# Kernel optimization log

Hardware: AMD Instinct MI355X
Metric: run time of the kernel (lower is better)

Reference implementation:

```python
import jax, jax.numpy as jnp
import numpy as np

EMBED = 1024
B, S = 8, 2048

def setup_inputs() -> dict:
    key = jax.random.key(0)
    k1, k2 = jax.random.split(key)
    x = jax.random.normal(k1, (B, S, EMBED), dtype=jnp.float32)
    # torch Linear(embed, 3*embed): store weight already transposed as [E, 3E]
    W_qkv = jax.random.normal(k2, (EMBED, 3 * EMBED), dtype=jnp.float32) * (1.0 / np.sqrt(EMBED))
    b_qkv = jnp.zeros((3 * EMBED,), dtype=jnp.float32)
    return {"x": x, "W_qkv": W_qkv, "b_qkv": b_qkv}

def reference(x, W_qkv, b_qkv):
    E = x.shape[-1]
    qkv = x @ W_qkv + b_qkv                      # [B,S,3E]
    Q, K, V = jnp.split(qkv, 3, axis=-1)         # each [B,S,E]
    scale = 1.0 / jnp.sqrt(jnp.asarray(E, x.dtype))
    scores = jnp.einsum('bqe,bke->bqk', Q, K) * scale  # [B,S,S]
    attn = jax.nn.softmax(scores, axis=-1)
    return jnp.einsum('bqk,bke->bqe', attn, V)   # [B,S,E]
```

## Files before the change

kernel.cpp:

```cpp
#include <hip/hip_runtime.h>

typedef unsigned short u16;
typedef unsigned int u32;
typedef __attribute__((ext_vector_type(8))) short short8;
typedef __attribute__((ext_vector_type(4))) short short4v;
typedef __attribute__((ext_vector_type(4))) float f32x4;

__device__ __forceinline__ u16 f2bf(float f) {
    u32 u = __float_as_uint(f);
    u32 r = (u + 0x7fffu + ((u >> 16) & 1u)) >> 16;
    return (u16)r;
}
__device__ __forceinline__ float bf2f(u16 h) {
    return __uint_as_float(((u32)h) << 16);
}

__device__ __forceinline__ void gload_lds16(const void* g, void* l) {
    __builtin_amdgcn_global_load_lds((const __attribute__((address_space(1))) void*)g,
                                     (__attribute__((address_space(3))) void*)l, 16, 0, 0);
}

#define BARRIER() do { __builtin_amdgcn_sched_barrier(0); __builtin_amdgcn_s_barrier(); __builtin_amdgcn_sched_barrier(0); } while (0)
#define VMCNT(N)  asm volatile("s_waitcnt vmcnt(" #N ")" ::: "memory")

#define STAGE(ptr, LDG, LOFF, RBASE, kelem) \
    do { gload_lds16((ptr) + (size_t)(RBASE) * (LDG) + (kelem),        lds + (LOFF) + ((RBASE) + (wid << 3)) * 128); \
         gload_lds16((ptr) + (size_t)((RBASE) + 64) * (LDG) + (kelem), lds + (LOFF) + ((RBASE) + 64 + (wid << 3)) * 128); } while (0)

template<int ROFF, int QH>
__device__ __forceinline__ void ld_a(short8 (&a)[4][2], const char* lds, int arow, int c0, int c1) {
    #pragma unroll
    for (int mf = 0; mf < 4; ++mf) {
        a[mf][0] = *(const short8*)(lds + ROFF + QH * 16384 + mf * 2048 + arow + c0);
        a[mf][1] = *(const short8*)(lds + ROFF + QH * 16384 + mf * 2048 + arow + c1);
    }
}
template<int ROFF, int QH>
__device__ __forceinline__ void ld_b(short8 (&b)[2][2], const char* lds, int brow, int c0, int c1) {
    #pragma unroll
    for (int nf = 0; nf < 2; ++nf) {
        b[nf][0] = *(const short8*)(lds + ROFF + QH * 16384 + nf * 2048 + brow + c0);
        b[nf][1] = *(const short8*)(lds + ROFF + QH * 16384 + nf * 2048 + brow + c1);
    }
}

template<int QM, int QN>
__device__ __forceinline__ void mfq(f32x4 (&acc)[2][4][2][2], short8 (&a)[4][2], short8 (&b)[2][2]) {
    __builtin_amdgcn_s_setprio(1);
    #pragma unroll
    for (int mf = 0; mf < 4; ++mf)
        #pragma unroll
        for (int nf = 0; nf < 2; ++nf) {
            acc[QM][mf][QN][nf] = __builtin_amdgcn_mfma_f32_16x16x32_bf16(a[mf][0], b[nf][0], acc[QM][mf][QN][nf], 0, 0, 0);
            acc[QM][mf][QN][nf] = __builtin_amdgcn_mfma_f32_16x16x32_bf16(a[mf][1], b[nf][1], acc[QM][mf][QN][nf], 0, 0, 0);
        }
    __builtin_amdgcn_s_setprio(0);
}

template<int EPI, int LDA, int LDB, int LDC, int K>
__global__ __launch_bounds__(512, 2)
void gemm8p(const u16* __restrict__ A, long long sA,
            const u16* __restrict__ B, long long sB,
            void* __restrict__ Cv, long long sC,
            const float* __restrict__ bias, float* __restrict__ ps,
            u16* __restrict__ vt, float scale, int GX, int GY)
{
    extern __shared__ char lds[];
    const int tid  = threadIdx.x;
    const int wid  = tid >> 6;
    const int lane = tid & 63;

    const int nwg = gridDim.x;
    int bid = blockIdx.x;
    bid = (bid & 7) * (nwg >> 3) + (bid >> 3);
    const int bx  = bid % GX;
    const int rem = bid / GX;
    const int by  = rem % GY;
    const long long z = rem / GY;

    const int bm = by * 256, bn = bx * 256;
    const u16* Atile = A + z * sA + (size_t)bm * LDA;
    const u16* Btile = B + z * sB + (size_t)bn * LDB;

    const int wm = wid >> 2, wn = wid & 3;
    const int l15   = lane & 15;
    const int lxor  = (lane & 7) << 4;
    const int khi   = (lane >> 4) << 4;
    const int colk0 = khi ^ lxor;
    const int colk1 = (64 + khi) ^ lxor;
    const int arow  = (wm * 64 + l15) * 128;
    const int brow  = (wn * 32 + l15) * 128;

    const int swz = ((lane & 7) ^ (lane >> 3)) << 3;
    const u16* pA = Atile + (size_t)((wid << 3) + (lane >> 3)) * LDA + swz;
    const u16* pB = Btile + (size_t)((wid << 3) + (lane >> 3)) * LDB + swz;

    f32x4 acc[2][4][2][2];
    #pragma unroll
    for (int i = 0; i < 2; ++i)
        #pragma unroll
        for (int m = 0; m < 4; ++m)
            #pragma unroll
            for (int j = 0; j < 2; ++j)
                #pragma unroll
                for (int n = 0; n < 2; ++n)
                    acc[i][m][j][n] = (f32x4){0.f, 0.f, 0.f, 0.f};

    STAGE(pA, LDA, 0,     0,   0);  STAGE(pA, LDA, 0,     128, 0);
    STAGE(pB, LDB, 32768, 0,   0);  STAGE(pB, LDB, 32768, 128, 0);
    STAGE(pA, LDA, 65536, 0,   64);
    STAGE(pB, LDB, 98304, 0,   64); STAGE(pB, LDB, 98304, 128, 64);
    VMCNT(6);
    BARRIER();

    short8 a[4][2], b0[2][2], b1[2][2];
    const int NI = K >> 7;

    for (int it = 0; it < NI; ++it) {
        const bool more = (it + 1 < NI);
        const int kc1 = it * 128 + 64;
        const int kn  = it * 128 + 128;
        const int kn2 = kn + 64;

        ld_a<0, 0>(a, lds, arow, colk0, colk1);
        ld_b<32768, 0>(b0, lds, brow, colk0, colk1);
        STAGE(pA, LDA, 65536, 128, kc1);
        BARRIER(); mfq<0, 0>(acc, a, b0);
        ld_b<32768, 1>(b1, lds, brow, colk0, colk1);
        BARRIER(); mfq<0, 1>(acc, a, b1);
        ld_a<0, 1>(a, lds, arow, colk0, colk1);
        if (more) STAGE(pB, LDB, 32768, 0, kn);
        BARRIER(); mfq<1, 1>(acc, a, b1);
        if (more) { STAGE(pB, LDB, 32768, 128, kn); VMCNT(4); }
        else      { VMCNT(0); }
        BARRIER(); mfq<1, 0>(acc, a, b0);
        ld_a<65536, 0>(a, lds, arow, colk0, colk1);
        ld_b<98304, 0>(b0, lds, brow, colk0, colk1);
        if (more) STAGE(pA, LDA, 0, 0, kn);
        BARRIER(); mfq<0, 0>(acc, a, b0);
        ld_b<98304, 1>(b1, lds, brow, colk0, colk1);
        if (more) STAGE(pA, LDA, 0, 128, kn);
        BARRIER(); mfq<0, 1>(acc, a, b1);
        ld_a<65536, 1>(a, lds, arow, colk0, colk1);
        if (more) { STAGE(pB, LDB, 98304, 0, kn2); STAGE(pB, LDB, 98304, 128, kn2); }
        BARRIER(); mfq<1, 1>(acc, a, b1);
        if (more) STAGE(pA, LDA, 65536, 0, kn2);
        VMCNT(6);
        BARRIER(); mfq<1, 0>(acc, a, b0);
    }

    const int r0 = (lane >> 4) * 4;
    const int cc = lane & 15;

    if (EPI == 3) {
        BARRIER();
        float* rs = (float*)lds;
        u16* C = (u16*)Cv + z * sC;
        float rsum[2][4][4];
        #pragma unroll
        for (int qm = 0; qm < 2; ++qm)
            #pragma unroll
            for (int mf = 0; mf < 4; ++mf)
                #pragma unroll
                for (int r = 0; r < 4; ++r) rsum[qm][mf][r] = 0.f;
        #pragma unroll
        for (int qn = 0; qn < 2; ++qn)
            #pragma unroll
            for (int nf = 0; nf < 2; ++nf) {
                const int col = bn + qn * 128 + wn * 32 + nf * 16 + cc;
                #pragma unroll
                for (int qm = 0; qm < 2; ++qm)
                    #pragma unroll
                    for (int mf = 0; mf < 4; ++mf) {
                        const int row = bm + qm * 128 + wm * 64 + mf * 16 + r0;
                        #pragma unroll
                        for (int r = 0; r < 4; ++r) {
                            const float e = __expf(acc[qm][mf][qn][nf][r] * scale);
                            const u16 eb = f2bf(e);
                            C[(size_t)(row + r) * LDC + col] = eb;
                            rsum[qm][mf][r] += bf2f(eb);
                        }
                    }
            }
        #pragma unroll
        for (int qm = 0; qm < 2; ++qm)
            #pragma unroll
            for (int mf = 0; mf < 4; ++mf)
                #pragma unroll
                for (int r = 0; r < 4; ++r) {
                    float v = rsum[qm][mf][r];
                    v += __shfl_xor(v, 1); v += __shfl_xor(v, 2);
                    v += __shfl_xor(v, 4); v += __shfl_xor(v, 8);
                    if (cc == 0)
                        rs[wn * 256 + qm * 128 + wm * 64 + mf * 16 + r0 + r] = v;
                }
        __syncthreads();
        if (tid < 256) {
            const float s = rs[tid] + rs[256 + tid] + rs[512 + tid] + rs[768 + tid];
            ps[((size_t)z * 2048 + bm + tid) * GX + bx] = s;
        }
        return;
    }

    if (EPI == 4) {
        BARRIER();
        float* di = (float*)lds;
        if (tid < 256) {
            const float* p = ps + ((size_t)z * 2048 + bm + tid) * 8;
            const float s = ((p[0] + p[1]) + (p[2] + p[3])) + ((p[4] + p[5]) + (p[6] + p[7]));
            di[tid] = 1.0f / s;
        }
        __syncthreads();
        float* C = (float*)Cv + z * sC;
        #pragma unroll
        for (int qn = 0; qn < 2; ++qn)
            #pragma unroll
            for (int nf = 0; nf < 2; ++nf) {
                const int col = bn + qn * 128 + wn * 32 + nf * 16 + cc;
                #pragma unroll
                for (int qm = 0; qm < 2; ++qm)
                    #pragma unroll
                    for (int mf = 0; mf < 4; ++mf) {
                        const int ro = qm * 128 + wm * 64 + mf * 16 + r0;
                        #pragma unroll
                        for (int r = 0; r < 4; ++r)
                            C[(size_t)(bm + ro + r) * LDC + col] = acc[qm][mf][qn][nf][r] * di[ro + r];
                    }
            }
        return;
    }

    if (EPI == 0 && bn >= 2048) {
        #pragma unroll
        for (int qn = 0; qn < 2; ++qn)
            #pragma unroll
            for (int nf = 0; nf < 2; ++nf) {
                const int col = bn + qn * 128 + wn * 32 + nf * 16 + cc;
                const float badd = bias[col];
                const int e = col - 2048;
                #pragma unroll
                for (int qm = 0; qm < 2; ++qm)
                    #pragma unroll
                    for (int mf = 0; mf < 4; ++mf) {
                        const int row = bm + qm * 128 + wm * 64 + mf * 16 + r0;
                        short4v o;
                        #pragma unroll
                        for (int r = 0; r < 4; ++r)
                            o[r] = (short)f2bf(acc[qm][mf][qn][nf][r] + badd);
                        *(short4v*)&vt[((size_t)(row >> 11) << 21) + (size_t)e * 2048 + (row & 2047)] = o;
                    }
            }
        return;
    }

    #pragma unroll
    for (int qn = 0; qn < 2; ++qn)
        #pragma unroll
        for (int nf = 0; nf < 2; ++nf) {
            const int col = bn + qn * 128 + wn * 32 + nf * 16 + cc;
            const float badd = bias[col];
            #pragma unroll
            for (int qm = 0; qm < 2; ++qm)
                #pragma unroll
                for (int mf = 0; mf < 4; ++mf) {
                    const int row = bm + qm * 128 + wm * 64 + mf * 16 + r0;
                    #pragma unroll
                    for (int r = 0; r < 4; ++r) {
                        const float v = acc[qm][mf][qn][nf][r] + badd;
                        ((u16*)Cv + z * sC)[(size_t)(row + r) * LDC + col] = f2bf(v);
                    }
                }
        }
}

__global__ __launch_bounds__(256)
void cvt_fused(const float* __restrict__ x, u16* __restrict__ xb,
               const float* __restrict__ W, u16* __restrict__ Wt)
{
    __shared__ u16 T[32][33];
    const int blk = blockIdx.x;
    const int tid = threadIdx.x;
    if (blk < 4096) {
        const float4* p = (const float4*)x;
        const int i0 = blk * 256 + tid;
        float4 a0 = p[2 * i0],             b0v = p[2 * i0 + 1];
        float4 a1 = p[2 * (i0 + 1048576)], b1v = p[2 * (i0 + 1048576) + 1];
        short8 o0, o1;
        o0[0] = (short)f2bf(a0.x); o0[1] = (short)f2bf(a0.y);
        o0[2] = (short)f2bf(a0.z); o0[3] = (short)f2bf(a0.w);
        o0[4] = (short)f2bf(b0v.x); o0[5] = (short)f2bf(b0v.y);
        o0[6] = (short)f2bf(b0v.z); o0[7] = (short)f2bf(b0v.w);
        o1[0] = (short)f2bf(a1.x); o1[1] = (short)f2bf(a1.y);
        o1[2] = (short)f2bf(a1.z); o1[3] = (short)f2bf(a1.w);
        o1[4] = (short)f2bf(b1v.x); o1[5] = (short)f2bf(b1v.y);
        o1[6] = (short)f2bf(b1v.z); o1[7] = (short)f2bf(b1v.w);
        ((short8*)xb)[i0] = o0;
        ((short8*)xb)[i0 + 1048576] = o1;
        return;
    }
    const int wb = blk - 4096;
    const int c0 = (wb % 96) * 32;
    const int r0 = (wb / 96) * 32;
    const int tr = tid >> 3;
    const int tc = (tid & 7) * 4;
    const float4 v = *(const float4*)&W[(size_t)(r0 + tr) * 3072 + c0 + tc];
    T[tr][tc + 0] = f2bf(v.x); T[tr][tc + 1] = f2bf(v.y);
    T[tr][tc + 2] = f2bf(v.z); T[tr][tc + 3] = f2bf(v.w);
    __syncthreads();
    short4v o;
    o[0] = (short)T[tc + 0][tr]; o[1] = (short)T[tc + 1][tr];
    o[2] = (short)T[tc + 2][tr]; o[3] = (short)T[tc + 3][tr];
    *(short4v*)&Wt[(size_t)(c0 + tr) * 1024 + r0 + tc] = o;
}

extern "C" void kernel_launch(void* const* d_in, const int* in_sizes, int n_in,
                              void* d_out, int out_size, void* d_ws, size_t ws_size,
                              hipStream_t stream) {
    const float* x    = (const float*)d_in[0];
    const float* W    = (const float*)d_in[1];
    const float* bias = (const float*)d_in[2];
    float* out = (float*)d_out;

    const int B = 8, S = 2048, E = 1024, N3 = 3072;
    const int M = B * S;

    char* ws = (char*)d_ws;
    u16* xb   = (u16*)ws;
    u16* Wtb  = (u16*)(ws + 33554432);
    u16* qkvb = (u16*)(ws + 39845888);
    u16* Vtb  = (u16*)(ws + 140509184);
    u16* Sb   = (u16*)(ws + 174063616);

    const size_t sbFull = (size_t)B * S * S * 2;
    const size_t sbOne  = (size_t)S * S * 2;
    const size_t psFull = (size_t)M * 8 * sizeof(float);
    const size_t need_full = 174063616ull + sbFull + psFull;
    const bool full = ws_size >= need_full;

    float* Ps = (float*)(ws + 174063616 + (full ? sbFull : sbOne));

    const float sc = 1.0f / 32.0f;
    const int LDSB = 131072;

    auto kQKV = gemm8p<0, 1024, 1024, 3072, 1024>;
    auto kQKT = gemm8p<3, 3072, 3072, 2048, 1024>;
    auto kPV  = gemm8p<4, 2048, 2048, 1024, 2048>;
    (void)hipFuncSetAttribute(reinterpret_cast<const void*>(kQKV),
                              hipFuncAttributeMaxDynamicSharedMemorySize, LDSB);
    (void)hipFuncSetAttribute(reinterpret_cast<const void*>(kQKT),
                              hipFuncAttributeMaxDynamicSharedMemorySize, LDSB);
    (void)hipFuncSetAttribute(reinterpret_cast<const void*>(kPV),
                              hipFuncAttributeMaxDynamicSharedMemorySize, LDSB);

    cvt_fused<<<dim3(7168), 256, 0, stream>>>(x, xb, W, Wtb);

    kQKV<<<dim3(12 * 64), 512, LDSB, stream>>>(xb, 0, Wtb, 0, qkvb, 0,
                                               bias, nullptr, Vtb, 1.0f, 12, 64);

    if (full) {
        kQKT<<<dim3(8 * 8 * 8), 512, LDSB, stream>>>(
            qkvb, (long long)S * N3, qkvb + E, (long long)S * N3,
            Sb, (long long)S * S, nullptr, Ps, nullptr, sc, 8, 8);
        kPV<<<dim3(4 * 8 * 8), 512, LDSB, stream>>>(
            Sb, (long long)S * S, Vtb, (long long)E * S,
            out, (long long)S * E, nullptr, Ps, nullptr, 1.0f, 4, 8);
    } else {
        for (int b = 0; b < B; ++b) {
            const u16* Qb = qkvb + (size_t)b * S * N3;
            kQKT<<<dim3(8 * 8), 512, LDSB, stream>>>(
                Qb, 0, Qb + E, 0, Sb, 0, nullptr, Ps, nullptr, sc, 8, 8);
            kPV<<<dim3(4 * 8), 512, LDSB, stream>>>(
                Sb, 0, Vtb + (size_t)b * E * S, 0,
                out + (size_t)b * S * E, 0, nullptr, Ps, nullptr, 1.0f, 4, 8);
        }
    }
}
```

Measured before the change: 258.9 us.

## Shrink GEMM tiles to 256x128 with double-buffered register/LDS pipeline

All three GEMMs move from 256x256 output tiles to 256x128 tiles. Each wave now owns a 64x64 sub-tile, which halves the accumulator registers and doubles the grid size, and the per-row partial-sum buffer for the softmax grows from 8 to 16 columns. The main loop is rebuilt as a two-stage double buffer: register fragments for the next half are loaded while MFMAs run on the current one, with explicit lgkmcnt and vmcnt waits, and LDS use drops to 96KB. The aim is better occupancy and latency hiding, at the cost of lower arithmetic intensity per tile and more global traffic for the shared operand.

```diff
diff --git a/kernel.cpp b/kernel.cpp
--- a/kernel.cpp
+++ b/kernel.cpp
@@ -22,44 +22,45 @@
 
 #define BARRIER() do { __builtin_amdgcn_sched_barrier(0); __builtin_amdgcn_s_barrier(); __builtin_amdgcn_sched_barrier(0); } while (0)
 #define VMCNT(N)  asm volatile("s_waitcnt vmcnt(" #N ")" ::: "memory")
+#define LGKM0     asm volatile("s_waitcnt lgkmcnt(0)" ::: "memory")
 
 #define STAGE(ptr, LDG, LOFF, RBASE, kelem) \
     do { gload_lds16((ptr) + (size_t)(RBASE) * (LDG) + (kelem),        lds + (LOFF) + ((RBASE) + (wid << 3)) * 128); \
          gload_lds16((ptr) + (size_t)((RBASE) + 64) * (LDG) + (kelem), lds + (LOFF) + ((RBASE) + 64 + (wid << 3)) * 128); } while (0)
 
-template<int ROFF, int QH>
-__device__ __forceinline__ void ld_a(short8 (&a)[4][2], const char* lds, int arow, int c0, int c1) {
+template<int OFF>
+__device__ __forceinline__ void ld_a4(short8 (&a)[4][2], const char* lds, int arow, int c0, int c1) {
     #pragma unroll
     for (int mf = 0; mf < 4; ++mf) {
-        a[mf][0] = *(const short8*)(lds + ROFF + QH * 16384 + mf * 2048 + arow + c0);
-        a[mf][1] = *(const short8*)(lds + ROFF + QH * 16384 + mf * 2048 + arow + c1);
-    }
-}
-template<int ROFF, int QH>
-__device__ __forceinline__ void ld_b(short8 (&b)[2][2], const char* lds, int brow, int c0, int c1) {
-    #pragma unroll
-    for (int nf = 0; nf < 2; ++nf) {
-        b[nf][0] = *(const short8*)(lds + ROFF + QH * 16384 + nf * 2048 + brow + c0);
-        b[nf][1] = *(const short8*)(lds + ROFF + QH * 16384 + nf * 2048 + brow + c1);
-    }
-}
-
-template<int QM, int QN>
-__device__ __forceinline__ void mfq(f32x4 (&acc)[2][4][2][2], short8 (&a)[4][2], short8 (&b)[2][2]) {
+        a[mf][0] = *(const short8*)(lds + OFF + mf * 2048 + arow + c0);
+        a[mf][1] = *(const short8*)(lds + OFF + mf * 2048 + arow + c1);
+    }
+}
+template<int OFF>
+__device__ __forceinline__ void ld_b4(short8 (&b)[4][2], const char* lds, int brow, int c0, int c1) {
+    #pragma unroll
+    for (int nf = 0; nf < 4; ++nf) {
+        b[nf][0] = *(const short8*)(lds + OFF + nf * 2048 + brow + c0);
+        b[nf][1] = *(const short8*)(lds + OFF + nf * 2048 + brow + c1);
+    }
+}
+
+template<int NF0>
+__device__ __forceinline__ void mfq2(f32x4 (&acc)[4][4], short8 (&a)[4][2], short8 (&b)[4][2]) {
     __builtin_amdgcn_s_setprio(1);
     #pragma unroll
     for (int mf = 0; mf < 4; ++mf)
         #pragma unroll
-        for (int nf = 0; nf < 2; ++nf) {
-            acc[QM][mf][QN][nf] = __builtin_amdgcn_mfma_f32_16x16x32_bf16(a[mf][0], b[nf][0], acc[QM][mf][QN][nf], 0, 0, 0);
-            acc[QM][mf][QN][nf] = __builtin_amdgcn_mfma_f32_16x16x32_bf16(a[mf][1], b[nf][1], acc[QM][mf][QN][nf], 0, 0, 0);
+        for (int nf = NF0; nf < NF0 + 2; ++nf) {
+            acc[mf][nf] = __builtin_amdgcn_mfma_f32_16x16x32_bf16(a[mf][0], b[nf][0], acc[mf][nf], 0, 0, 0);
+            acc[mf][nf] = __builtin_amdgcn_mfma_f32_16x16x32_bf16(a[mf][1], b[nf][1], acc[mf][nf], 0, 0, 0);
         }
     __builtin_amdgcn_s_setprio(0);
 }
 
 template<int EPI, int LDA, int LDB, int LDC, int K>
 __global__ __launch_bounds__(512, 2)
-void gemm8p(const u16* __restrict__ A, long long sA,
+void gemmdb(const u16* __restrict__ A, long long sA,
             const u16* __restrict__ B, long long sB,
             void* __restrict__ Cv, long long sC,
             const float* __restrict__ bias, float* __restrict__ ps,
@@ -78,75 +79,62 @@
     const int by  = rem % GY;
     const long long z = rem / GY;
 
-    const int bm = by * 256, bn = bx * 256;
+    const int bm = by * 256, bn = bx * 128;
     const u16* Atile = A + z * sA + (size_t)bm * LDA;
     const u16* Btile = B + z * sB + (size_t)bn * LDB;
 
-    const int wm = wid >> 2, wn = wid & 3;
+    const int wm = wid >> 1, wn = wid & 1;
     const int l15   = lane & 15;
     const int lxor  = (lane & 7) << 4;
     const int khi   = (lane >> 4) << 4;
     const int colk0 = khi ^ lxor;
     const int colk1 = (64 + khi) ^ lxor;
     const int arow  = (wm * 64 + l15) * 128;
-    const int brow  = (wn * 32 + l15) * 128;
+    const int brow  = (wn * 64 + l15) * 128;
 
     const int swz = ((lane & 7) ^ (lane >> 3)) << 3;
     const u16* pA = Atile + (size_t)((wid << 3) + (lane >> 3)) * LDA + swz;
     const u16* pB = Btile + (size_t)((wid << 3) + (lane >> 3)) * LDB + swz;
 
-    f32x4 acc[2][4][2][2];
-    #pragma unroll
-    for (int i = 0; i < 2; ++i)
-        #pragma unroll
-        for (int m = 0; m < 4; ++m)
-            #pragma unroll
-            for (int j = 0; j < 2; ++j)
-                #pragma unroll
-                for (int n = 0; n < 2; ++n)
-                    acc[i][m][j][n] = (f32x4){0.f, 0.f, 0.f, 0.f};
-
-    STAGE(pA, LDA, 0,     0,   0);  STAGE(pA, LDA, 0,     128, 0);
-    STAGE(pB, LDB, 32768, 0,   0);  STAGE(pB, LDB, 32768, 128, 0);
-    STAGE(pA, LDA, 65536, 0,   64);
-    STAGE(pB, LDB, 98304, 0,   64); STAGE(pB, LDB, 98304, 128, 64);
+    f32x4 acc[4][4];
+    #pragma unroll
+    for (int m = 0; m < 4; ++m)
+        #pragma unroll
+        for (int n = 0; n < 4; ++n)
+            acc[m][n] = (f32x4){0.f, 0.f, 0.f, 0.f};
+
+    STAGE(pA, LDA, 0,     0,   0); STAGE(pA, LDA, 0,     128, 0); STAGE(pB, LDB, 32768, 0, 0);
+    STAGE(pA, LDA, 49152, 0,  64); STAGE(pA, LDA, 49152, 128, 64); STAGE(pB, LDB, 81920, 0, 64);
     VMCNT(6);
     BARRIER();
 
-    short8 a[4][2], b0[2][2], b1[2][2];
+    short8 aX[4][2], bX[4][2], aY[4][2], bY[4][2];
+    ld_a4<0>(aX, lds, arow, colk0, colk1);
+    ld_b4<32768>(bX, lds, brow, colk0, colk1);
+    VMCNT(0);
+    LGKM0;
+    BARRIER();
+
     const int NI = K >> 7;
 
     for (int it = 0; it < NI; ++it) {
         const bool more = (it + 1 < NI);
-        const int kc1 = it * 128 + 64;
         const int kn  = it * 128 + 128;
         const int kn2 = kn + 64;
 
-        ld_a<0, 0>(a, lds, arow, colk0, colk1);
-        ld_b<32768, 0>(b0, lds, brow, colk0, colk1);
-        STAGE(pA, LDA, 65536, 128, kc1);
-        BARRIER(); mfq<0, 0>(acc, a, b0);
-        ld_b<32768, 1>(b1, lds, brow, colk0, colk1);
-        BARRIER(); mfq<0, 1>(acc, a, b1);
-        ld_a<0, 1>(a, lds, arow, colk0, colk1);
-        if (more) STAGE(pB, LDB, 32768, 0, kn);
-        BARRIER(); mfq<1, 1>(acc, a, b1);
-        if (more) { STAGE(pB, LDB, 32768, 128, kn); VMCNT(4); }
-        else      { VMCNT(0); }
-        BARRIER(); mfq<1, 0>(acc, a, b0);
-        ld_a<65536, 0>(a, lds, arow, colk0, colk1);
-        ld_b<98304, 0>(b0, lds, brow, colk0, colk1);
-        if (more) STAGE(pA, LDA, 0, 0, kn);
-        BARRIER(); mfq<0, 0>(acc, a, b0);
-        ld_b<98304, 1>(b1, lds, brow, colk0, colk1);
-        if (more) STAGE(pA, LDA, 0, 128, kn);
-        BARRIER(); mfq<0, 1>(acc, a, b1);
-        ld_a<65536, 1>(a, lds, arow, colk0, colk1);
-        if (more) { STAGE(pB, LDB, 98304, 0, kn2); STAGE(pB, LDB, 98304, 128, kn2); }
-        BARRIER(); mfq<1, 1>(acc, a, b1);
-        if (more) STAGE(pA, LDA, 65536, 0, kn2);
+        ld_a4<49152>(aY, lds, arow, colk0, colk1);
+        ld_b4<81920>(bY, lds, brow, colk0, colk1);
+        if (more) { STAGE(pA, LDA, 0, 0, kn); STAGE(pA, LDA, 0, 128, kn); STAGE(pB, LDB, 32768, 0, kn); }
+        LGKM0;
+        BARRIER(); mfq2<0>(acc, aX, bX);
+        if (more) { STAGE(pA, LDA, 49152, 0, kn2); STAGE(pA, LDA, 49152, 128, kn2); STAGE(pB, LDB, 81920, 0, kn2); }
         VMCNT(6);
-        BARRIER(); mfq<1, 0>(acc, a, b0);
+        BARRIER(); mfq2<2>(acc, aX, bX);
+        if (more) { ld_a4<0>(aX, lds, arow, colk0, colk1); ld_b4<32768>(bX, lds, brow, colk0, colk1); }
+        LGKM0;
+        BARRIER(); mfq2<0>(acc, aY, bY);
+        VMCNT(0);
+        BARRIER(); mfq2<2>(acc, aY, bY);
     }
 
     const int r0 = (lane >> 4) * 4;
@@ -156,47 +144,39 @@
         BARRIER();
         float* rs = (float*)lds;
         u16* C = (u16*)Cv + z * sC;
-        float rsum[2][4][4];
-        #pragma unroll
-        for (int qm = 0; qm < 2; ++qm)
-            #pragma unroll
-            for (int mf = 0; mf < 4; ++mf)
-                #pragma unroll
-                for (int r = 0; r < 4; ++r) rsum[qm][mf][r] = 0.f;
-        #pragma unroll
-        for (int qn = 0; qn < 2; ++qn)
-            #pragma unroll
-            for (int nf = 0; nf < 2; ++nf) {
-                const int col = bn + qn * 128 + wn * 32 + nf * 16 + cc;
-                #pragma unroll
-                for (int qm = 0; qm < 2; ++qm)
-                    #pragma unroll
-                    for (int mf = 0; mf < 4; ++mf) {
-                        const int row = bm + qm * 128 + wm * 64 + mf * 16 + r0;
-                        #pragma unroll
-                        for (int r = 0; r < 4; ++r) {
-                            const float e = __expf(acc[qm][mf][qn][nf][r] * scale);
-                            const u16 eb = f2bf(e);
-                            C[(size_t)(row + r) * LDC + col] = eb;
-                            rsum[qm][mf][r] += bf2f(eb);
-                        }
-                    }
-            }
-        #pragma unroll
-        for (int qm = 0; qm < 2; ++qm)
-            #pragma unroll
-            for (int mf = 0; mf < 4; ++mf)
+        float rsum[4][4];
+        #pragma unroll
+        for (int mf = 0; mf < 4; ++mf)
+            #pragma unroll
+            for (int r = 0; r < 4; ++r) rsum[mf][r] = 0.f;
+        #pragma unroll
+        for (int nf = 0; nf < 4; ++nf) {
+            const int col = bn + wn * 64 + nf * 16 + cc;
+            #pragma unroll
+            for (int mf = 0; mf < 4; ++mf) {
+                const int row = bm + wm * 64 + mf * 16 + r0;
                 #pragma unroll
                 for (int r = 0; r < 4; ++r) {
-                    float v = rsum[qm][mf][r];
-                    v += __shfl_xor(v, 1); v += __shfl_xor(v, 2);
-                    v += __shfl_xor(v, 4); v += __shfl_xor(v, 8);
-                    if (cc == 0)
-                        rs[wn * 256 + qm * 128 + wm * 64 + mf * 16 + r0 + r] = v;
+                    const float e = __expf(acc[mf][nf][r] * scale);
+                    const u16 eb = f2bf(e);
+                    C[(size_t)(row + r) * LDC + col] = eb;
+                    rsum[mf][r] += bf2f(eb);
                 }
+            }
+        }
+        #pragma unroll
+        for (int mf = 0; mf < 4; ++mf)
+            #pragma unroll
+            for (int r = 0; r < 4; ++r) {
+                float v = rsum[mf][r];
+                v += __shfl_xor(v, 1); v += __shfl_xor(v, 2);
+                v += __shfl_xor(v, 4); v += __shfl_xor(v, 8);
+                if (cc == 0)
+                    rs[wn * 256 + wm * 64 + mf * 16 + r0 + r] = v;
+            }
         __syncthreads();
         if (tid < 256) {
-            const float s = rs[tid] + rs[256 + tid] + rs[512 + tid] + rs[768 + tid];
+            const float s = rs[tid] + rs[256 + tid];
             ps[((size_t)z * 2048 + bm + tid) * GX + bx] = s;
         }
         return;
@@ -206,71 +186,60 @@
         BARRIER();
         float* di = (float*)lds;
         if (tid < 256) {
-            const float* p = ps + ((size_t)z * 2048 + bm + tid) * 8;
-            const float s = ((p[0] + p[1]) + (p[2] + p[3])) + ((p[4] + p[5]) + (p[6] + p[7]));
+            const float* p = ps + ((size_t)z * 2048 + bm + tid) * 16;
+            float s = 0.f;
+            #pragma unroll
+            for (int j = 0; j < 16; j += 4)
+                s += ((p[j] + p[j + 1]) + (p[j + 2] + p[j + 3]));
             di[tid] = 1.0f / s;
         }
         __syncthreads();
         float* C = (float*)Cv + z * sC;
         #pragma unroll
-        for (int qn = 0; qn < 2; ++qn)
-            #pragma unroll
-            for (int nf = 0; nf < 2; ++nf) {
-                const int col = bn + qn * 128 + wn * 32 + nf * 16 + cc;
+        for (int nf = 0; nf < 4; ++nf) {
+            const int col = bn + wn * 64 + nf * 16 + cc;
+            #pragma unroll
+            for (int mf = 0; mf < 4; ++mf) {
+                const int ro = wm * 64 + mf * 16 + r0;
                 #pragma unroll
-                for (int qm = 0; qm < 2; ++qm)
-                    #pragma unroll
-                    for (int mf = 0; mf < 4; ++mf) {
-                        const int ro = qm * 128 + wm * 64 + mf * 16 + r0;
-                        #pragma unroll
-                        for (int r = 0; r < 4; ++r)
-                            C[(size_t)(bm + ro + r) * LDC + col] = acc[qm][mf][qn][nf][r] * di[ro + r];
-                    }
+                for (int r = 0; r < 4; ++r)
+                    C[(size_t)(bm + ro + r) * LDC + col] = acc[mf][nf][r] * di[ro + r];
             }
+        }
         return;
     }
 
     if (EPI == 0 && bn >= 2048) {
         #pragma unroll
-        for (int qn = 0; qn < 2; ++qn)
-            #pragma unroll
-            for (int nf = 0; nf < 2; ++nf) {
-                const int col = bn + qn * 128 + wn * 32 + nf * 16 + cc;
-                const float badd = bias[col];
-                const int e = col - 2048;
+        for (int nf = 0; nf < 4; ++nf) {
+            const int col = bn + wn * 64 + nf * 16 + cc;
+            const float badd = bias[col];
+            const int e = col - 2048;
+            #pragma unroll
+            for (int mf = 0; mf < 4; ++mf) {
+                const int row = bm + wm * 64 + mf * 16 + r0;
+                short4v o;
                 #pragma unroll
-                for (int qm = 0; qm < 2; ++qm)
-                    #pragma unroll
-                    for (int mf = 0; mf < 4; ++mf) {
-                        const int row = bm + qm * 128 + wm * 64 + mf * 16 + r0;
-                        short4v o;
-                        #pragma unroll
-                        for (int r = 0; r < 4; ++r)
-                            o[r] = (short)f2bf(acc[qm][mf][qn][nf][r] + badd);
-                        *(short4v*)&vt[((size_t)(row >> 11) << 21) + (size_t)e * 2048 + (row & 2047)] = o;
-                    }
+                for (int r = 0; r < 4; ++r)
+                    o[r] = (short)f2bf(acc[mf][nf][r] + badd);
+                *(short4v*)&vt[((size_t)(row >> 11) << 21) + (size_t)e * 2048 + (row & 2047)] = o;
             }
+        }
         return;
     }
 
     #pragma unroll
-    for (int qn = 0; qn < 2; ++qn)
-        #pragma unroll
-        for (int nf = 0; nf < 2; ++nf) {
-            const int col = bn + qn * 128 + wn * 32 + nf * 16 + cc;
-            const float badd = bias[col];
-            #pragma unroll
-            for (int qm = 0; qm < 2; ++qm)
-                #pragma unroll
-                for (int mf = 0; mf < 4; ++mf) {
-                    const int row = bm + qm * 128 + wm * 64 + mf * 16 + r0;
-                    #pragma unroll
-                    for (int r = 0; r < 4; ++r) {
-                        const float v = acc[qm][mf][qn][nf][r] + badd;
-                        ((u16*)Cv + z * sC)[(size_t)(row + r) * LDC + col] = f2bf(v);
-                    }
-                }
-        }
+    for (int nf = 0; nf < 4; ++nf) {
+        const int col = bn + wn * 64 + nf * 16 + cc;
+        const float badd = bias[col];
+        #pragma unroll
+        for (int mf = 0; mf < 4; ++mf) {
+            const int row = bm + wm * 64 + mf * 16 + r0;
+            #pragma unroll
+            for (int r = 0; r < 4; ++r)
+                ((u16*)Cv + z * sC)[(size_t)(row + r) * LDC + col] = f2bf(acc[mf][nf][r] + badd);
+        }
+    }
 }
 
 __global__ __launch_bounds__(256)
@@ -333,18 +302,18 @@
 
     const size_t sbFull = (size_t)B * S * S * 2;
     const size_t sbOne  = (size_t)S * S * 2;
-    const size_t psFull = (size_t)M * 8 * sizeof(float);
+    const size_t psFull = (size_t)M * 16 * sizeof(float);
     const size_t need_full = 174063616ull + sbFull + psFull;
     const bool full = ws_size >= need_full;
 
     float* Ps = (float*)(ws + 174063616 + (full ? sbFull : sbOne));
 
     const float sc = 1.0f / 32.0f;
-    const int LDSB = 131072;
-
-    auto kQKV = gemm8p<0, 1024, 1024, 3072, 1024>;
-    auto kQKT = gemm8p<3, 3072, 3072, 2048, 1024>;
-    auto kPV  = gemm8p<4, 2048, 2048, 1024, 2048>;
+    const int LDSB = 98304;
+
+    auto kQKV = gemmdb<0, 1024, 1024, 3072, 1024>;
+    auto kQKT = gemmdb<3, 3072, 3072, 2048, 1024>;
+    auto kPV  = gemmdb<4, 2048, 2048, 1024, 2048>;
     (void)hipFuncSetAttribute(reinterpret_cast<const void*>(kQKV),
                               hipFuncAttributeMaxDynamicSharedMemorySize, LDSB);
     (void)hipFuncSetAttribute(reinterpret_cast<const void*>(kQKT),
@@ -354,24 +323,24 @@
 
     cvt_fused<<<dim3(7168), 256, 0, stream>>>(x, xb, W, Wtb);
 
-    kQKV<<<dim3(12 * 64), 512, LDSB, stream>>>(xb, 0, Wtb, 0, qkvb, 0,
-                                               bias, nullptr, Vtb, 1.0f, 12, 64);
+    kQKV<<<dim3(24 * 64), 512, LDSB, stream>>>(xb, 0, Wtb, 0, qkvb, 0,
+                                               bias, nullptr, Vtb, 1.0f, 24, 64);
 
     if (full) {
-        kQKT<<<dim3(8 * 8 * 8), 512, LDSB, stream>>>(
+        kQKT<<<dim3(16 * 8 * 8), 512, LDSB, stream>>>(
             qkvb, (long long)S * N3, qkvb + E, (long long)S * N3,
-            Sb, (long long)S * S, nullptr, Ps, nullptr, sc, 8, 8);
-        kPV<<<dim3(4 * 8 * 8), 512, LDSB, stream>>>(
+            Sb, (long long)S * S, nullptr, Ps, nullptr, sc, 16, 8);
+        kPV<<<dim3(8 * 8 * 8), 512, LDSB, stream>>>(
             Sb, (long long)S * S, Vtb, (long long)E * S,
-            out, (long long)S * E, nullptr, Ps, nullptr, 1.0f, 4, 8);
+            out, (long long)S * E, nullptr, Ps, nullptr, 1.0f, 8, 8);
     } else {
         for (int b = 0; b < B; ++b) {
             const u16* Qb = qkvb + (size_t)b * S * N3;
-            kQKT<<<dim3(8 * 8), 512, LDSB, stream>>>(
-                Qb, 0, Qb + E, 0, Sb, 0, nullptr, Ps, nullptr, sc, 8, 8);
-            kPV<<<dim3(4 * 8), 512, LDSB, stream>>>(
+            kQKT<<<dim3(16 * 8), 512, LDSB, stream>>>(
+                Qb, 0, Qb + E, 0, Sb, 0, nullptr, Ps, nullptr, sc, 16, 8);
+            kPV<<<dim3(8 * 8), 512, LDSB, stream>>>(
                 Sb, 0, Vtb + (size_t)b * E * S, 0,
-                out + (size_t)b * S * E, 0, nullptr, Ps, nullptr, 1.0f, 4, 8);
-        }
-    }
-}
+                out + (size_t)b * S * E, 0, nullptr, Ps, nullptr, 1.0f, 8, 8);
+        }
+    }
+}
```

New measurement: 306.7 us. 18.4% more time.
